# Kernel tuning notes

Measured on AMD Instinct MI355X. Metric: run time of the kernel, lower is better.

Reference implementation:

```python
import jax, jax.numpy as jnp
import numpy as np
import math

B, S, D, H = 2, 2048, 1024, 16
HD = D // H  # head dim = 64


def _rope_tables():
    # RoFormer sinusoidal position embedding: one frequency per (even, odd) pair
    pos = jnp.arange(S, dtype=jnp.float32)[:, None]                # [S, 1]
    inv_freq = 1.0 / (10000.0 ** (jnp.arange(0, HD, 2, dtype=jnp.float32) / HD))  # [HD/2]
    ang = pos * inv_freq[None, :]                                   # [S, HD/2]
    sin = jnp.sin(ang)[None, None]                                  # [1,1,S,HD/2]
    cos = jnp.cos(ang)[None, None]
    return sin, cos


def setup_inputs() -> dict:
    key = jax.random.key(0)
    k0, k1, k2, k3 = jax.random.split(key, 4)
    scale = 1.0 / math.sqrt(D)
    sin, cos = _rope_tables()
    return {
        "hidden_states": jax.random.normal(k0, (B, S, D), dtype=jnp.float32),
        "Wq": jax.random.normal(k1, (D, D), dtype=jnp.float32) * scale,
        "Wk": jax.random.normal(k2, (D, D), dtype=jnp.float32) * scale,
        "Wv": jax.random.normal(k3, (D, D), dtype=jnp.float32) * scale,
        "sin": sin,
        "cos": cos,
    }


def _split_heads(x):
    # [B,S,D] -> [B,H,S,HD]
    b, s, _ = x.shape
    return x.reshape(b, s, H, HD).transpose(0, 2, 1, 3)


def _apply_rotary(x, sin, cos):
    # x: [B,H,S,HD]; sin/cos broadcast as [1,1,S,HD/2]
    x1 = x[..., 0::2]
    x2 = x[..., 1::2]
    out = jnp.stack([x1 * cos - x2 * sin, x2 * cos + x1 * sin], axis=-1)
    return out.reshape(x.shape)


def reference(hidden_states, Wq, Wk, Wv, sin, cos):
    q = _apply_rotary(_split_heads(hidden_states @ Wq), sin, cos)  # [B,H,S,HD]
    k = _apply_rotary(_split_heads(hidden_states @ Wk), sin, cos)
    v = _apply_rotary(_split_heads(hidden_states @ Wv), sin, cos)  # note: RoPE on V too, per source
    scores = jnp.einsum("bhqd,bhkd->bhqk", q, k) / math.sqrt(HD)   # [B,H,S,S]
    probs = jax.nn.softmax(scores, axis=-1)
    ctx = jnp.einsum("bhqk,bhkd->bhqd", probs, v)                   # [B,H,S,HD]
    return ctx.transpose(0, 2, 1, 3).reshape(hidden_states.shape[0], S, D)
```

## Files before the change

kernel.cpp:

```cpp
#include <hip/hip_runtime.h>

typedef unsigned short u16;
typedef unsigned short u16x8 __attribute__((ext_vector_type(8)));
typedef unsigned short u16x4 __attribute__((ext_vector_type(4)));
typedef short s16x4 __attribute__((ext_vector_type(4)));
typedef __bf16 bf16x8_t __attribute__((ext_vector_type(8)));
typedef float floatx4 __attribute__((ext_vector_type(4)));

#define BATCH 2
#define S_LEN 2048
#define D_DIM 1024
#define NH    16
#define HD    64

__device__ __forceinline__ u16 f2b(float f) {
  union { float f; unsigned int i; } c; c.f = f;
  const unsigned int i = c.i;
  return (u16)((i + 0x7FFFu + ((i >> 16) & 1u)) >> 16);
}
__device__ __forceinline__ unsigned int fbits(float f) {
  union { float f; unsigned int i; } c; c.f = f; return c.i;
}
__device__ __forceinline__ bf16x8_t asbf(u16x8 v) {
  union { u16x8 u; bf16x8_t b; } c; c.u = v; return c.b;
}
__device__ __forceinline__ s16x4 as4(uint2 v) {
  union { uint2 u; s16x4 s; } c; c.u = v; return c.s;
}
__device__ __forceinline__ s16x4 as4u(u16x4 v) {
  union { u16x4 u; s16x4 s; } c; c.u = v; return c.s;
}
__device__ __forceinline__ void load_lds16(const u16* g, u16* l) {
  __builtin_amdgcn_global_load_lds(
      (const __attribute__((address_space(1))) void*)g,
      (__attribute__((address_space(3))) void*)l, 16, 0, 0);
}

__device__ __attribute__((aligned(256))) u16 g_xb[(size_t)BATCH * S_LEN * D_DIM];
__device__ __attribute__((aligned(256))) u16 g_wt[3u * D_DIM * D_DIM];
__device__ __attribute__((aligned(256))) u16 g_qkv[3u * BATCH * S_LEN * D_DIM];

__global__ __launch_bounds__(256) void prep(const float* __restrict__ X,
                                            const float* __restrict__ Wq,
                                            const float* __restrict__ Wk,
                                            const float* __restrict__ Wv) {
  const int tid = threadIdx.x;
  const int z = blockIdx.y;
  if (z == 3) {
#pragma unroll
    for (int c = 0; c < 8; ++c) {
      const size_t i = (((size_t)c * 256 + blockIdx.x) * 256 + tid) * 8;
      floatx4 a = *(const floatx4*)(X + i);
      floatx4 b = *(const floatx4*)(X + i + 4);
      u16x8 o;
#pragma unroll
      for (int j = 0; j < 4; ++j) { o[j] = f2b(a[j]); o[4 + j] = f2b(b[j]); }
      *(u16x8*)(g_xb + i) = o;
    }
    return;
  }
  __shared__ u16 t[64][65];
  const float* W = (z == 0) ? Wq : (z == 1) ? Wk : Wv;
  u16* Wt = g_wt + (size_t)z * D_DIM * D_DIM;
  const int k0 = (blockIdx.x & 15) * 64;
  const int n0 = (blockIdx.x >> 4) * 64;
  const int rr = tid >> 4;
  const int cc = (tid & 15) * 4;
#pragma unroll
  for (int i = 0; i < 4; ++i) {
    const int r = rr + i * 16;
    floatx4 v = *(const floatx4*)(W + (size_t)(k0 + r) * D_DIM + n0 + cc);
    t[r][cc] = f2b(v[0]); t[r][cc + 1] = f2b(v[1]);
    t[r][cc + 2] = f2b(v[2]); t[r][cc + 3] = f2b(v[3]);
  }
  __syncthreads();
#pragma unroll
  for (int i = 0; i < 4; ++i) {
    const int r = rr + i * 16;
    u16x4 v;
    v[0] = t[cc][r]; v[1] = t[cc + 1][r]; v[2] = t[cc + 2][r]; v[3] = t[cc + 3][r];
    *(u16x4*)(Wt + (size_t)(n0 + r) * D_DIM + k0 + cc) = v;
  }
}

__global__ __launch_bounds__(256) void qkv_gemm(const float* __restrict__ sin_t,
                                                const float* __restrict__ cos_t) {
  __shared__ __attribute__((aligned(16))) u16 lds_a[128 * 32];
  __shared__ __attribute__((aligned(16))) u16 lds_b[128 * 32];
  const int tid = threadIdx.x;
  const int wv = tid >> 6;
  const int lane = tid & 63;
  const int lrow = lane & 15;
  const int quad = lane >> 4;
  const int wr = wv >> 1, wc = wv & 1;
  const int m0 = blockIdx.x * 128;
  const int n0 = blockIdx.y * 128;
  const int z = blockIdx.z;
  const bool vmode = (z == 2);
  const u16* Wz = g_wt + (size_t)z * (D_DIM * D_DIM);

  floatx4 acc[4][4] = {};

  const u16* gA = g_xb + (size_t)(m0 + wv * 32 + (lane >> 2)) * D_DIM + (lane & 3) * 8;
  const u16* gB = Wz   + (size_t)(n0 + wv * 32 + (lane >> 2)) * D_DIM + (lane & 3) * 8;
  u16* sA = &lds_a[(wv * 32) * 32];
  u16* sB = &lds_b[(wv * 32) * 32];

  const u16* Aarr = vmode ? lds_a : lds_b;
  const u16* Barr = vmode ? lds_b : lds_a;

  for (int k0 = 0; k0 < D_DIM; k0 += 32) {
    __syncthreads();
    load_lds16(gA + k0, sA);
    load_lds16(gA + (size_t)16 * D_DIM + k0, sA + 512);
    load_lds16(gB + k0, sB);
    load_lds16(gB + (size_t)16 * D_DIM + k0, sB + 512);
    __syncthreads();
    u16x8 af[4], bfr[4];
#pragma unroll
    for (int mi = 0; mi < 4; ++mi)
      af[mi] = *(const u16x8*)&Aarr[(wr * 64 + mi * 16 + lrow) * 32 + quad * 8];
#pragma unroll
    for (int ni = 0; ni < 4; ++ni)
      bfr[ni] = *(const u16x8*)&Barr[(wc * 64 + ni * 16 + lrow) * 32 + quad * 8];
#pragma unroll
    for (int mi = 0; mi < 4; ++mi)
#pragma unroll
      for (int ni = 0; ni < 4; ++ni)
        acc[mi][ni] = __builtin_amdgcn_mfma_f32_16x16x32_bf16(
            asbf(af[mi]), asbf(bfr[ni]), acc[mi][ni], 0, 0, 0);
  }

  if (!vmode) {
    const float qsc = (z == 0) ? 0.18033688011112042f : 1.0f;
    u16* outz = g_qkv + (size_t)z * (BATCH * S_LEN * D_DIM);
#pragma unroll
    for (int mi = 0; mi < 4; ++mi) {
      const int nf0 = n0 + wr * 64 + mi * 16 + quad * 4;
      const int h = nf0 >> 6, hd0 = nf0 & 63, i00 = hd0 >> 1;
#pragma unroll
      for (int ni = 0; ni < 4; ++ni) {
        const int sg = m0 + wc * 64 + ni * 16 + lrow;
        const int b = sg >> 11, srow = sg & 2047;
        const float c0 = cos_t[(size_t)srow * 32 + i00];
        const float s0 = sin_t[(size_t)srow * 32 + i00];
        const float c1 = cos_t[(size_t)srow * 32 + i00 + 1];
        const float s1 = sin_t[(size_t)srow * 32 + i00 + 1];
        const float v0 = acc[mi][ni][0], v1 = acc[mi][ni][1];
        const float v2 = acc[mi][ni][2], v3 = acc[mi][ni][3];
        u16x4 ov;
        ov[0] = f2b((v0 * c0 - v1 * s0) * qsc);
        ov[1] = f2b((v1 * c0 + v0 * s0) * qsc);
        ov[2] = f2b((v2 * c1 - v3 * s1) * qsc);
        ov[3] = f2b((v3 * c1 + v2 * s1) * qsc);
        *(u16x4*)(outz + ((size_t)(b * NH + h) * S_LEN + srow) * HD + hd0) = ov;
      }
    }
  } else {
    u16* outv = g_qkv + (size_t)2 * (BATCH * S_LEN * D_DIM);
#pragma unroll
    for (int mi = 0; mi < 4; ++mi) {
      const int s0g = m0 + wr * 64 + mi * 16 + quad * 4;
      const int b = s0g >> 11, sl = s0g & 2047;
#pragma unroll
      for (int ni = 0; ni < 4; ++ni) {
        const int nf = n0 + wc * 64 + ni * 16 + lrow;
        const int h = nf >> 6, hd = nf & 63, i0 = hd >> 1;
        const float sgn = (hd & 1) ? 1.f : -1.f;
        u16x4 ov;
#pragma unroll
        for (int r = 0; r < 4; ++r) {
          const int s = sl + r;
          const float c  = cos_t[(size_t)s * 32 + i0];
          const float sn = sin_t[(size_t)s * 32 + i0];
          const float v  = acc[mi][ni][r];
          const float vp = __shfl_xor(v, 1);
          ov[r] = f2b(v * c + sgn * sn * vp);
        }
        *(u16x4*)(outv + (size_t)(b * NH + h) * (S_LEN * HD) +
                  ((size_t)(sl >> 2) * HD + hd) * 4) = ov;
      }
    }
  }
}

#define VP 260
__global__ __launch_bounds__(256) void flash_attn(float* __restrict__ out) {
  __shared__ __attribute__((aligned(16))) u16 lds_k[2][128 * 72];
  __shared__ __attribute__((aligned(16))) u16 lds_v[2][32 * VP];
  const int bh = blockIdx.x;
  const int qt = blockIdx.y;
  const int b = bh >> 4, h = bh & 15;
  const int tid = threadIdx.x, wv = tid >> 6, lane = tid & 63;
  const int lrow = lane & 15, quad = lane >> 4;
  const u16* Qb = g_qkv + (size_t)bh * (S_LEN * HD);
  const u16* Kb = g_qkv + (size_t)(BATCH * NH + bh) * (S_LEN * HD);
  const u16* Vb = g_qkv + (size_t)(2 * BATCH * NH + bh) * (S_LEN * HD);
  const int q0 = qt * 128 + wv * 32;

  u16x8 qf[2][2];
#pragma unroll
  for (int qb = 0; qb < 2; ++qb)
#pragma unroll
    for (int ks = 0; ks < 2; ++ks)
      qf[qb][ks] = *(const u16x8*)(Qb + (size_t)(q0 + qb * 16 + lrow) * HD +
                                   ks * 32 + quad * 8);

  floatx4 oacc[2][4] = {};
  float l_part[2] = {};

  const int krow = tid >> 1;
  const int kcol = (tid & 1) * 32;

  u16x8 kreg[4], vreg[4];
#pragma unroll
  for (int i = 0; i < 4; ++i)
    kreg[i] = *(const u16x8*)(Kb + (size_t)krow * HD + kcol + i * 8);
#pragma unroll
  for (int c = 0; c < 4; ++c)
    vreg[c] = *(const u16x8*)(Vb + (size_t)c * 2048 + tid * 8);

  for (int t = 0; t < S_LEN / 128; ++t) {
    const int buf = t & 1;
#pragma unroll
    for (int i = 0; i < 4; ++i)
      *(u16x8*)&lds_k[buf][krow * 72 + kcol + i * 8] = kreg[i];
#pragma unroll
    for (int c = 0; c < 4; ++c) {
      const int off = c * 2048 + tid * 8;
      *(u16x8*)&lds_v[buf][(off >> 8) * VP + (off & 255)] = vreg[c];
    }
    __syncthreads();
    if (t + 1 < S_LEN / 128) {
      const size_t kn = (size_t)(t + 1) * 128 * HD;
#pragma unroll
      for (int i = 0; i < 4; ++i)
        kreg[i] = *(const u16x8*)(Kb + kn + (size_t)krow * HD + kcol + i * 8);
#pragma unroll
      for (int c = 0; c < 4; ++c)
        vreg[c] = *(const u16x8*)(Vb + kn + (size_t)c * 2048 + tid * 8);
    }

#pragma unroll
    for (int sub = 0; sub < 2; ++sub) {
      u16x8 kf[4][2];
#pragma unroll
      for (int nb = 0; nb < 4; ++nb)
#pragma unroll
        for (int ks = 0; ks < 2; ++ks)
          kf[nb][ks] = *(const u16x8*)&lds_k[buf][(sub * 64 + nb * 16 + lrow) * 72 +
                                                 ks * 32 + quad * 8];
      u16x4 vf[4][4];
#pragma unroll
      for (int nb = 0; nb < 4; ++nb)
#pragma unroll
        for (int hb = 0; hb < 4; ++hb)
          vf[nb][hb] = *(const u16x4*)&lds_v[buf][(sub * 16 + nb * 4 + quad) * VP +
                                                 (hb * 16 + lrow) * 4];

      floatx4 sacc[2][4];
      __builtin_amdgcn_s_setprio(1);
#pragma unroll
      for (int qb = 0; qb < 2; ++qb)
#pragma unroll
        for (int nb = 0; nb < 4; ++nb) {
          floatx4 s0 = {};
          s0 = __builtin_amdgcn_mfma_f32_16x16x32_bf16(
              asbf(kf[nb][0]), asbf(qf[qb][0]), s0, 0, 0, 0);
          sacc[qb][nb] = __builtin_amdgcn_mfma_f32_16x16x32_bf16(
              asbf(kf[nb][1]), asbf(qf[qb][1]), s0, 0, 0, 0);
        }
      __builtin_amdgcn_s_setprio(0);

      s16x4 pa[2][4];
#pragma unroll
      for (int qb = 0; qb < 2; ++qb)
#pragma unroll
        for (int nb = 0; nb < 4; ++nb) {
          const float p0 = __builtin_amdgcn_exp2f(sacc[qb][nb][0]);
          const float p1 = __builtin_amdgcn_exp2f(sacc[qb][nb][1]);
          const float p2 = __builtin_amdgcn_exp2f(sacc[qb][nb][2]);
          const float p3 = __builtin_amdgcn_exp2f(sacc[qb][nb][3]);
          l_part[qb] += (p0 + p1) + (p2 + p3);
          uint2 pk;
          pk.x = __byte_perm(fbits(p0), fbits(p1), 0x7632);
          pk.y = __byte_perm(fbits(p2), fbits(p3), 0x7632);
          pa[qb][nb] = as4(pk);
        }

      __builtin_amdgcn_s_setprio(1);
#pragma unroll
      for (int qb = 0; qb < 2; ++qb)
#pragma unroll
        for (int nb = 0; nb < 4; ++nb)
#pragma unroll
          for (int hb = 0; hb < 4; ++hb)
            oacc[qb][hb] = __builtin_amdgcn_mfma_f32_16x16x16bf16_1k(
                pa[qb][nb], as4u(vf[nb][hb]), oacc[qb][hb], 0, 0, 0);
      __builtin_amdgcn_s_setprio(0);
    }
  }

#pragma unroll
  for (int qb = 0; qb < 2; ++qb) {
    float l = l_part[qb];
    l += __shfl_xor(l, 16);
    l += __shfl_xor(l, 32);
    float linv[4];
#pragma unroll
    for (int r = 0; r < 4; ++r)
      linv[r] = 1.f / __shfl(l, quad * 4 + r);
#pragma unroll
    for (int hb = 0; hb < 4; ++hb) {
      const int hd = hb * 16 + lrow;
#pragma unroll
      for (int r = 0; r < 4; ++r) {
        const int q = q0 + qb * 16 + quad * 4 + r;
        out[((size_t)(b * S_LEN) + q) * D_DIM + h * HD + hd] =
            oacc[qb][hb][r] * linv[r];
      }
    }
  }
}

extern "C" void kernel_launch(void* const* d_in, const int* in_sizes, int n_in,
                              void* d_out, int out_size, void* d_ws, size_t ws_size,
                              hipStream_t stream) {
  const float* X = (const float*)d_in[0];
  const float* sin_t = (const float*)d_in[4];
  const float* cos_t = (const float*)d_in[5];

  prep<<<dim3(256, 4), 256, 0, stream>>>(X, (const float*)d_in[1],
                                         (const float*)d_in[2],
                                         (const float*)d_in[3]);

  qkv_gemm<<<dim3(32, 8, 3), 256, 0, stream>>>(sin_t, cos_t);

  flash_attn<<<dim3(32, 16), 256, 0, stream>>>((float*)d_out);
}
```

Before: 184.9 us.

## Store Q/K in 4-wide head-dim-interleaved layout and restage K LDS tiles

Changes the projection kernel's Q/K output layout from row-major [S,HD] to groups of 4 head-dim elements laid out across sequence positions, matching the layout already used for V. Flash attention now loads K tiles as 16 rows of 128 positions times 4 into a padded LDS buffer and builds MFMA fragments from two 8-byte reads. The aim is contiguous, coalesced K global loads and fewer LDS bank conflicts. In exchange, each fragment now needs two smaller LDS reads instead of one 16-byte read, and Q loads become strided 8-byte reads.

```diff
diff --git a/kernel.cpp b/kernel.cpp
--- a/kernel.cpp
+++ b/kernel.cpp
@@ -29,6 +29,12 @@
 }
 __device__ __forceinline__ s16x4 as4u(u16x4 v) {
   union { u16x4 u; s16x4 s; } c; c.u = v; return c.s;
+}
+__device__ __forceinline__ u16x8 cat44(u16x4 a, u16x4 b) {
+  u16x8 r;
+#pragma unroll
+  for (int i = 0; i < 4; ++i) { r[i] = a[i]; r[4 + i] = b[i]; }
+  return r;
 }
 __device__ __forceinline__ void load_lds16(const u16* g, u16* l) {
   __builtin_amdgcn_global_load_lds(
@@ -153,7 +159,8 @@
         ov[1] = f2b((v1 * c0 + v0 * s0) * qsc);
         ov[2] = f2b((v2 * c1 - v3 * s1) * qsc);
         ov[3] = f2b((v3 * c1 + v2 * s1) * qsc);
-        *(u16x4*)(outz + ((size_t)(b * NH + h) * S_LEN + srow) * HD + hd0) = ov;
+        *(u16x4*)(outz + (size_t)(b * NH + h) * (S_LEN * HD) +
+                  ((size_t)(hd0 >> 2) * S_LEN + srow) * 4) = ov;
       }
     }
   } else {
@@ -185,8 +192,9 @@
 }
 
 #define VP 260
+#define KP 520
 __global__ __launch_bounds__(256) void flash_attn(float* __restrict__ out) {
-  __shared__ __attribute__((aligned(16))) u16 lds_k[2][128 * 72];
+  __shared__ __attribute__((aligned(16))) u16 lds_k[2][16 * KP];
   __shared__ __attribute__((aligned(16))) u16 lds_v[2][32 * VP];
   const int bh = blockIdx.x;
   const int qt = blockIdx.y;
@@ -202,20 +210,23 @@
 #pragma unroll
   for (int qb = 0; qb < 2; ++qb)
 #pragma unroll
-    for (int ks = 0; ks < 2; ++ks)
-      qf[qb][ks] = *(const u16x8*)(Qb + (size_t)(q0 + qb * 16 + lrow) * HD +
-                                   ks * 32 + quad * 8);
+    for (int ks = 0; ks < 2; ++ks) {
+      const int q = q0 + qb * 16 + lrow;
+      const int j0 = ks * 8 + quad * 2;
+      qf[qb][ks] = cat44(
+          *(const u16x4*)(Qb + ((size_t)j0 * S_LEN + q) * 4),
+          *(const u16x4*)(Qb + ((size_t)(j0 + 1) * S_LEN + q) * 4));
+    }
 
   floatx4 oacc[2][4] = {};
   float l_part[2] = {};
 
-  const int krow = tid >> 1;
-  const int kcol = (tid & 1) * 32;
-
   u16x8 kreg[4], vreg[4];
 #pragma unroll
-  for (int i = 0; i < 4; ++i)
-    kreg[i] = *(const u16x8*)(Kb + (size_t)krow * HD + kcol + i * 8);
+  for (int i = 0; i < 4; ++i) {
+    const int u = i * 256 + tid, j = u >> 6, w = u & 63;
+    kreg[i] = *(const u16x8*)(Kb + (size_t)j * (S_LEN * 4) + w * 8);
+  }
 #pragma unroll
   for (int c = 0; c < 4; ++c)
     vreg[c] = *(const u16x8*)(Vb + (size_t)c * 2048 + tid * 8);
@@ -223,8 +234,10 @@
   for (int t = 0; t < S_LEN / 128; ++t) {
     const int buf = t & 1;
 #pragma unroll
-    for (int i = 0; i < 4; ++i)
-      *(u16x8*)&lds_k[buf][krow * 72 + kcol + i * 8] = kreg[i];
+    for (int i = 0; i < 4; ++i) {
+      const int u = i * 256 + tid, j = u >> 6, w = u & 63;
+      *(u16x8*)&lds_k[buf][j * KP + w * 8] = kreg[i];
+    }
 #pragma unroll
     for (int c = 0; c < 4; ++c) {
       const int off = c * 2048 + tid * 8;
@@ -232,13 +245,16 @@
     }
     __syncthreads();
     if (t + 1 < S_LEN / 128) {
-      const size_t kn = (size_t)(t + 1) * 128 * HD;
-#pragma unroll
-      for (int i = 0; i < 4; ++i)
-        kreg[i] = *(const u16x8*)(Kb + kn + (size_t)krow * HD + kcol + i * 8);
+#pragma unroll
+      for (int i = 0; i < 4; ++i) {
+        const int u = i * 256 + tid, j = u >> 6, w = u & 63;
+        kreg[i] = *(const u16x8*)(Kb + (size_t)j * (S_LEN * 4) +
+                                  (size_t)(t + 1) * 512 + w * 8);
+      }
+      const size_t vn = (size_t)(t + 1) * 128 * HD;
 #pragma unroll
       for (int c = 0; c < 4; ++c)
-        vreg[c] = *(const u16x8*)(Vb + kn + (size_t)c * 2048 + tid * 8);
+        vreg[c] = *(const u16x8*)(Vb + vn + (size_t)c * 2048 + tid * 8);
     }
 
 #pragma unroll
@@ -247,9 +263,13 @@
 #pragma unroll
       for (int nb = 0; nb < 4; ++nb)
 #pragma unroll
-        for (int ks = 0; ks < 2; ++ks)
-          kf[nb][ks] = *(const u16x8*)&lds_k[buf][(sub * 64 + nb * 16 + lrow) * 72 +
-                                                 ks * 32 + quad * 8];
+        for (int ks = 0; ks < 2; ++ks) {
+          const int j0 = ks * 8 + quad * 2;
+          const int ro = (sub * 64 + nb * 16 + lrow) * 4;
+          kf[nb][ks] = cat44(
+              *(const u16x4*)&lds_k[buf][j0 * KP + ro],
+              *(const u16x4*)&lds_k[buf][(j0 + 1) * KP + ro]);
+        }
       u16x4 vf[4][4];
 #pragma unroll
       for (int nb = 0; nb < 4; ++nb)
```

Result: no change. 187.1 us (+1.2%).
